# Optimization experiments

Measured on AMD Instinct MI355X. Metric: run time of the kernel, lower is better.

The kernel has to match this reference:

```python
import jax, jax.numpy as jnp
import numpy as np

SEQ = 16384
D = 1024


def setup_inputs() -> dict:
    key = jax.random.key(0)
    k1, k2, k3, k4 = jax.random.split(key, 4)
    return {
        "G_M1": jax.random.normal(k1, (SEQ, D), dtype=jnp.float32),
        "G_M2": jax.random.normal(k2, (SEQ, D), dtype=jnp.float32),
        "wp1": jax.random.normal(k3, (1, D), dtype=jnp.float32),
        "wp2": jax.random.normal(k4, (1, D), dtype=jnp.float32),
    }


def reference(G_M1, G_M2, wp1, wp2):
    # Original: per-row tensordot(wp1, G_M1[i][:, None]) -> [1,1], concat along
    # axis 1 -> p1 of shape [1, SEQ]; same for p2; softmax over the seq axis.
    # This is exactly a single matvec per head followed by softmax.
    p1 = jnp.einsum("od,sd->os", wp1, G_M1)  # [1, SEQ]
    p2 = jnp.einsum("od,sd->os", wp2, G_M2)  # [1, SEQ]
    p1_pred = jax.nn.softmax(p1, axis=-1)
    p2_pred = jax.nn.softmax(p2, axis=-1)
    return (p1_pred, p2_pred)
```

## Files before the change

### kernel.cpp

```cpp
#include <hip/hip_runtime.h>
#include <hip/hip_bf16.h>
#include <math.h>

#define SEQ 16384
#define D   1024
#define NBLK_DOT 8192

typedef float floatx4 __attribute__((ext_vector_type(4)));

__global__ __launch_bounds__(256) void dot_partial_kernel(
    const float* __restrict__ g1, const float* __restrict__ g2,
    const float* __restrict__ wp1, const float* __restrict__ wp2,
    float* __restrict__ logits,
    float* __restrict__ blk_m, float* __restrict__ blk_s) {
  const int lane = threadIdx.x & 63;
  const int wid  = threadIdx.x >> 6;
  const int r    = blockIdx.x * 4 + wid;
  const bool head1 = (blockIdx.x >= NBLK_DOT / 2);
  const float* g  = head1 ? g2 : g1;
  const float* wp = head1 ? wp2 : wp1;
  const int row   = head1 ? (r - SEQ) : r;

  floatx4 wv0 = *((const floatx4*)wp + lane);
  floatx4 wv1 = *((const floatx4*)wp + lane + 64);
  floatx4 wv2 = *((const floatx4*)wp + lane + 128);
  floatx4 wv3 = *((const floatx4*)wp + lane + 192);

  const floatx4* rv = (const floatx4*)(g + (size_t)row * D);
  floatx4 a0 = rv[lane];
  floatx4 a1 = rv[lane + 64];
  floatx4 a2 = rv[lane + 128];
  floatx4 a3 = rv[lane + 192];

  float acc = 0.f;
#pragma unroll
  for (int e = 0; e < 4; ++e) {
    acc = fmaf(a0[e], wv0[e], acc);
    acc = fmaf(a1[e], wv1[e], acc);
    acc = fmaf(a2[e], wv2[e], acc);
    acc = fmaf(a3[e], wv3[e], acc);
  }
#pragma unroll
  for (int off = 32; off > 0; off >>= 1)
    acc += __shfl_xor(acc, off, 64);

  if (lane == 0) logits[r] = acc;

  __shared__ float lv[4];
  if (lane == 0) lv[wid] = acc;
  __syncthreads();
  if (threadIdx.x == 0) {
    float M = fmaxf(fmaxf(lv[0], lv[1]), fmaxf(lv[2], lv[3]));
    float S = __expf(lv[0] - M) + __expf(lv[1] - M) +
              __expf(lv[2] - M) + __expf(lv[3] - M);
    blk_m[blockIdx.x] = M;
    blk_s[blockIdx.x] = S;
  }
}

__global__ __launch_bounds__(256) void finalize_kernel(
    const float* __restrict__ blk_m, const float* __restrict__ blk_s,
    const float4* __restrict__ logits4, float4* __restrict__ out4) {
  const int head = blockIdx.x >> 4;
  const int tid  = threadIdx.x;
  const int lane = tid & 63;
  const int wid  = tid >> 6;

  const float* pm = blk_m + head * (NBLK_DOT / 2) + tid * 16;
  const float* ps = blk_s + head * (NBLK_DOT / 2) + tid * 16;
  float M = -INFINITY, S = 0.f;
#pragma unroll
  for (int i = 0; i < 16; ++i) {
    float m = pm[i], s = ps[i];
    float nm = fmaxf(M, m);
    S = S * __expf(M - nm) + s * __expf(m - nm);
    M = nm;
  }
#pragma unroll
  for (int off = 32; off > 0; off >>= 1) {
    float m2 = __shfl_xor(M, off, 64);
    float s2 = __shfl_xor(S, off, 64);
    float nm = fmaxf(M, m2);
    S = S * __expf(M - nm) + s2 * __expf(m2 - nm);
    M = nm;
  }
  __shared__ float sm[4], ss[4], fin[2];
  if (lane == 0) { sm[wid] = M; ss[wid] = S; }
  __syncthreads();
  if (tid == 0) {
    float Mg = -INFINITY, Sg = 0.f;
#pragma unroll
    for (int i = 0; i < 4; ++i) {
      float nm = fmaxf(Mg, sm[i]);
      Sg = Sg * __expf(Mg - nm) + ss[i] * __expf(sm[i] - nm);
      Mg = nm;
    }
    fin[0] = Mg;
    fin[1] = 1.0f / Sg;
  }
  __syncthreads();
  const float Mg   = fin[0];
  const float invS = fin[1];

  const int i = head * 4096 + (blockIdx.x & 15) * 256 + tid;
  float4 v = logits4[i];
  float4 o;
  o.x = __expf(v.x - Mg) * invS;
  o.y = __expf(v.y - Mg) * invS;
  o.z = __expf(v.z - Mg) * invS;
  o.w = __expf(v.w - Mg) * invS;
  out4[i] = o;
}

extern "C" void kernel_launch(void* const* d_in, const int* in_sizes, int n_in,
                              void* d_out, int out_size, void* d_ws, size_t ws_size,
                              hipStream_t stream) {
  const float* g1  = (const float*)d_in[0];
  const float* g2  = (const float*)d_in[1];
  const float* wp1 = (const float*)d_in[2];
  const float* wp2 = (const float*)d_in[3];
  float* out = (float*)d_out;

  float* logits = (float*)d_ws;
  float* blk_m  = logits + 2 * SEQ;
  float* blk_s  = blk_m + NBLK_DOT;

  dot_partial_kernel<<<NBLK_DOT, 256, 0, stream>>>(g1, g2, wp1, wp2,
                                                   logits, blk_m, blk_s);
  finalize_kernel<<<32, 256, 0, stream>>>(blk_m, blk_s,
                                          (const float4*)logits, (float4*)out);
}
```

Baseline: 147.2 us.

## Process two rows per wave and drop block-level LDS reduction

Each wave now computes dot products for two consecutive rows, halving the block count and reusing the loaded weight vectors across both rows. The per-block shared-memory reduction and __syncthreads are removed; each wave writes its own (max, sum) pair as a float2 partial, and the finalize kernel reads 32 partials per thread instead of 16 separate max/sum values. This raises registers per thread and memory loads in flight per wave, at the cost of fewer waves overall.

```diff
diff --git a/kernel.cpp b/kernel.cpp
--- a/kernel.cpp
+++ b/kernel.cpp
@@ -4,76 +4,79 @@
 
 #define SEQ 16384
 #define D   1024
-#define NBLK_DOT 8192
+#define NBLK_DOT 4096
+#define NWAVES   16384
 
 typedef float floatx4 __attribute__((ext_vector_type(4)));
 
 __global__ __launch_bounds__(256) void dot_partial_kernel(
     const float* __restrict__ g1, const float* __restrict__ g2,
     const float* __restrict__ wp1, const float* __restrict__ wp2,
-    float* __restrict__ logits,
-    float* __restrict__ blk_m, float* __restrict__ blk_s) {
+    float* __restrict__ logits, float2* __restrict__ partials) {
   const int lane = threadIdx.x & 63;
   const int wid  = threadIdx.x >> 6;
-  const int r    = blockIdx.x * 4 + wid;
+  const int w    = blockIdx.x * 4 + wid;
+  const int r0   = w * 2;
   const bool head1 = (blockIdx.x >= NBLK_DOT / 2);
   const float* g  = head1 ? g2 : g1;
   const float* wp = head1 ? wp2 : wp1;
-  const int row   = head1 ? (r - SEQ) : r;
+  const int row0  = head1 ? (r0 - SEQ) : r0;
 
   floatx4 wv0 = *((const floatx4*)wp + lane);
   floatx4 wv1 = *((const floatx4*)wp + lane + 64);
   floatx4 wv2 = *((const floatx4*)wp + lane + 128);
   floatx4 wv3 = *((const floatx4*)wp + lane + 192);
 
-  const floatx4* rv = (const floatx4*)(g + (size_t)row * D);
+  const floatx4* rv = (const floatx4*)(g + (size_t)row0 * D);
   floatx4 a0 = rv[lane];
   floatx4 a1 = rv[lane + 64];
   floatx4 a2 = rv[lane + 128];
   floatx4 a3 = rv[lane + 192];
+  floatx4 b0 = rv[lane + 256];
+  floatx4 b1 = rv[lane + 320];
+  floatx4 b2 = rv[lane + 384];
+  floatx4 b3 = rv[lane + 448];
 
-  float acc = 0.f;
+  float acc0 = 0.f, acc1 = 0.f;
 #pragma unroll
   for (int e = 0; e < 4; ++e) {
-    acc = fmaf(a0[e], wv0[e], acc);
-    acc = fmaf(a1[e], wv1[e], acc);
-    acc = fmaf(a2[e], wv2[e], acc);
-    acc = fmaf(a3[e], wv3[e], acc);
+    acc0 = fmaf(a0[e], wv0[e], acc0);
+    acc0 = fmaf(a1[e], wv1[e], acc0);
+    acc0 = fmaf(a2[e], wv2[e], acc0);
+    acc0 = fmaf(a3[e], wv3[e], acc0);
+    acc1 = fmaf(b0[e], wv0[e], acc1);
+    acc1 = fmaf(b1[e], wv1[e], acc1);
+    acc1 = fmaf(b2[e], wv2[e], acc1);
+    acc1 = fmaf(b3[e], wv3[e], acc1);
   }
 #pragma unroll
-  for (int off = 32; off > 0; off >>= 1)
-    acc += __shfl_xor(acc, off, 64);
-
-  if (lane == 0) logits[r] = acc;
-
-  __shared__ float lv[4];
-  if (lane == 0) lv[wid] = acc;
-  __syncthreads();
-  if (threadIdx.x == 0) {
-    float M = fmaxf(fmaxf(lv[0], lv[1]), fmaxf(lv[2], lv[3]));
-    float S = __expf(lv[0] - M) + __expf(lv[1] - M) +
-              __expf(lv[2] - M) + __expf(lv[3] - M);
-    blk_m[blockIdx.x] = M;
-    blk_s[blockIdx.x] = S;
+  for (int off = 32; off > 0; off >>= 1) {
+    acc0 += __shfl_xor(acc0, off, 64);
+    acc1 += __shfl_xor(acc1, off, 64);
+  }
+  if (lane == 0) {
+    *(float2*)(logits + r0) = make_float2(acc0, acc1);
+    float mw = fmaxf(acc0, acc1);
+    float sw = __expf(acc0 - mw) + __expf(acc1 - mw);
+    partials[w] = make_float2(mw, sw);
   }
 }
 
 __global__ __launch_bounds__(256) void finalize_kernel(
-    const float* __restrict__ blk_m, const float* __restrict__ blk_s,
+    const float2* __restrict__ partials,
     const float4* __restrict__ logits4, float4* __restrict__ out4) {
   const int head = blockIdx.x >> 4;
   const int tid  = threadIdx.x;
   const int lane = tid & 63;
   const int wid  = tid >> 6;
 
-  const float* pm = blk_m + head * (NBLK_DOT / 2) + tid * 16;
-  const float* ps = blk_s + head * (NBLK_DOT / 2) + tid * 16;
+  const float2* pp = partials + head * (NWAVES / 2) + tid * 32;
   float M = -INFINITY, S = 0.f;
 #pragma unroll
-  for (int i = 0; i < 16; ++i) {
-    float m = pm[i], s = ps[i];
-    float nm = fmaxf(M, m);
-    S = S * __expf(M - nm) + s * __expf(m - nm);
+  for (int i = 0; i < 32; ++i) {
+    float2 p = pp[i];
+    float nm = fmaxf(M, p.x);
+    S = S * __expf(M - nm) + p.y * __expf(p.x - nm);
     M = nm;
   }
 #pragma unroll
@@ -121,12 +124,11 @@
   const float* wp2 = (const float*)d_in[3];
   float* out = (float*)d_out;
 
-  float* logits = (float*)d_ws;
-  float* blk_m  = logits + 2 * SEQ;
-  float* blk_s  = blk_m + NBLK_DOT;
+  float*  logits   = (float*)d_ws;
+  float2* partials = (float2*)(logits + 2 * SEQ);
 
   dot_partial_kernel<<<NBLK_DOT, 256, 0, stream>>>(g1, g2, wp1, wp2,
-                                                   logits, blk_m, blk_s);
-  finalize_kernel<<<32, 256, 0, stream>>>(blk_m, blk_s,
+                                                   logits, partials);
+  finalize_kernel<<<32, 256, 0, stream>>>(partials,
                                           (const float4*)logits, (float4*)out);
 }
```

Result: no change. 148.9 us (+1.2%).
